# Optimization experiments

Hardware: AMD Instinct MI355X
Metric: run time of the kernel (lower is better)

## Reference

```python
import jax, jax.numpy as jnp
import numpy as np

B = 8192      # batch_size
D = 1024      # d_model
E = 8         # num_domains
OUT = 2       # binary fake/real logits


def setup_inputs() -> dict:
    key = jax.random.key(0)
    k_feat, k_ids, k_w1, k_b1, k_w2, k_b2 = jax.random.split(key, 6)
    feature = jax.random.normal(k_feat, (B, D), dtype=jnp.float32)
    domain_ids = jax.random.randint(k_ids, (B,), 0, E, dtype=jnp.int64)
    # Per-domain expert parameters (torch Linear init ~ U(-1/sqrt(fan_in), 1/sqrt(fan_in)))
    s1 = 1.0 / np.sqrt(D)
    W1 = jax.random.uniform(k_w1, (E, D, D), jnp.float32, -s1, s1)   # acts as x @ W1[e]
    b1 = jax.random.uniform(k_b1, (E, D), jnp.float32, -s1, s1)
    W2 = jax.random.uniform(k_w2, (E, D, OUT), jnp.float32, -s1, s1)
    b2 = jax.random.uniform(k_b2, (E, OUT), jnp.float32, -s1, s1)
    return {"feature": feature, "domain_ids": domain_ids,
            "W1": W1, "b1": b1, "W2": W2, "b2": b2}


def reference(feature, domain_ids, W1, b1, W2, b2):
    # Eval-mode forward (Dropout is identity at inference).
    # Layer 1: compute for all E experts (E is small), then select per sample.
    # h_all: [B, E, D]
    h_all = jnp.einsum('bd,edh->beh', feature, W1)
    sel = jnp.arange(feature.shape[0])
    h = h_all[sel, domain_ids] + b1[domain_ids]          # [B, D]
    h = jax.nn.relu(h)
    # Layer 2: gather the tiny [D, 2] head per sample.
    logits = jnp.einsum('bd,bdo->bo', h, W2[domain_ids]) + b2[domain_ids]  # [B, 2]
    return logits
```

## Files before the change

### kernel.cpp

```cpp
#include <hip/hip_runtime.h>
#include <hip/hip_bf16.h>

#define NB 8192
#define ND 1024
#define NE 8
#define BSTRIDE 2048

typedef unsigned short u16;
typedef __bf16 bf16x8 __attribute__((ext_vector_type(8)));
typedef float f32x4 __attribute__((ext_vector_type(4)));
typedef u16 u16x8 __attribute__((ext_vector_type(8)));
typedef u16 u16x4 __attribute__((ext_vector_type(4)));

__device__ __forceinline__ u16 f2bf(float f) {
    union { float f; unsigned u; } v; v.f = f;
    unsigned r = v.u + 0x7fffu + ((v.u >> 16) & 1u);
    return (u16)(r >> 16);
}

__global__ __launch_bounds__(256) void k_pre(
    const float* __restrict__ X, u16* __restrict__ Xb,
    const float* __restrict__ W1, u16* __restrict__ W1t,
    const int* __restrict__ ids, const float* __restrict__ b2,
    float* __restrict__ out, int* __restrict__ counts, int* __restrict__ bucket)
{
    int bid = blockIdx.x;
    int t = threadIdx.x;
    if (bid < 4096) {
        long i = ((long)bid * 256 + t) * 8;
        f32x4 a = *(const f32x4*)(X + i);
        f32x4 b = *(const f32x4*)(X + i + 4);
        u16x8 o;
        o[0] = f2bf(a[0]); o[1] = f2bf(a[1]); o[2] = f2bf(a[2]); o[3] = f2bf(a[3]);
        o[4] = f2bf(b[0]); o[5] = f2bf(b[1]); o[6] = f2bf(b[2]); o[7] = f2bf(b[3]);
        *(u16x8*)(Xb + i) = o;
        return;
    }
    if (bid < 6144) {
        __shared__ float s[64][65];
        int bid2 = bid - 4096;
        int e = bid2 >> 8;
        int tr = ((bid2 >> 4) & 15) << 6;
        int tc = (bid2 & 15) << 6;
        const float* src = W1 + (size_t)e * ND * ND;
        u16* dst = W1t + (size_t)e * ND * ND;
        #pragma unroll
        for (int i = 0; i < 4; ++i) {
            int idx = i * 256 + t;
            int r = idx >> 4, c4 = (idx & 15) * 4;
            f32x4 v = *(const f32x4*)(src + (size_t)(tr + r) * ND + tc + c4);
            s[c4 + 0][r] = v[0]; s[c4 + 1][r] = v[1];
            s[c4 + 2][r] = v[2]; s[c4 + 3][r] = v[3];
        }
        __syncthreads();
        #pragma unroll
        for (int i = 0; i < 4; ++i) {
            int idx = i * 256 + t;
            int n = idx >> 4, k4 = (idx & 15) * 4;
            u16x4 o;
            o[0] = f2bf(s[n][k4 + 0]); o[1] = f2bf(s[n][k4 + 1]);
            o[2] = f2bf(s[n][k4 + 2]); o[3] = f2bf(s[n][k4 + 3]);
            *(u16x4*)(dst + (size_t)(tc + n) * ND + tr + k4) = o;
        }
        return;
    }
    int b = (bid - 6144) * 256 + t;
    int e = ids[b];
    out[2 * b]     = b2[2 * e];
    out[2 * b + 1] = b2[2 * e + 1];
    int lane = t & 63;
    unsigned long long lt = (1ull << lane) - 1ull;
    int pos = 0;
    #pragma unroll
    for (int ee = 0; ee < NE; ++ee) {
        unsigned long long m = __ballot(e == ee);
        if (m) {
            int leader = __ffsll((long long)m) - 1;
            int r = __popcll(m & lt);
            int base = 0;
            if (e == ee && r == 0) base = atomicAdd(&counts[ee], __popcll(m));
            base = __shfl(base, leader, 64);
            if (e == ee) pos = base + r;
        }
    }
    bucket[e * BSTRIDE + pos] = b;
}

#define GLDS16(src, dst) __builtin_amdgcn_global_load_lds( \
    (const __attribute__((address_space(1))) void*)(src), \
    (__attribute__((address_space(3))) void*)(dst), 16, 0, 0)

__global__ __launch_bounds__(256) void k_gemm(
    const u16* __restrict__ Xb, const u16* __restrict__ W1t,
    const float* __restrict__ b1, const float* __restrict__ W2,
    const int* __restrict__ counts, const int* __restrict__ bucket,
    float* __restrict__ out)
{
    __shared__ u16 sA[2][2048];
    __shared__ u16 sB[2][4096];
    __shared__ int sRows[64];

    int bid = blockIdx.x;
    int e  = bid & 7;
    int nt = (bid >> 3) & 7;
    int mt = bid >> 6;

    int cnt = counts[e];
    if (mt * 64 >= cnt) return;
    int rem = cnt - mt * 64;

    int t = threadIdx.x;
    if (t < 64) {
        int r = mt * 64 + t;
        sRows[t] = bucket[e * BSTRIDE + (r < cnt ? r : 0)];
    }
    __syncthreads();

    int n0 = nt * 128;
    int ar = t >> 2, as = (t & 3) * 8;
    const u16* ap  = Xb + (size_t)sRows[ar] * ND + as;
    const u16* b0p = W1t + ((size_t)e * ND + n0 + ar) * ND + as;
    const u16* b1p = W1t + ((size_t)e * ND + n0 + 64 + ar) * ND + as;
    int w = t >> 6;
    int l = t & 63;
    int lc = l & 15, kg = l >> 4;
    int wm = (w >> 1) * 32, wn = (w & 1) * 64;

    f32x4 acc[2][4] = {};

    char* A0 = (char*)sA;
    char* B0 = (char*)sB;

    auto stage = [&](int buf, int kt) {
        int k0 = kt * 32;
        GLDS16(ap  + k0, A0 + buf * 4096 + w * 1024);
        GLDS16(b0p + k0, B0 + buf * 8192 + w * 1024);
        GLDS16(b1p + k0, B0 + buf * 8192 + 4096 + w * 1024);
    };

    stage(0, 0);

    #pragma unroll 2
    for (int kt = 0; kt < 32; ++kt) {
        int buf = kt & 1;
        if (kt + 1 < 32) {
            stage(buf ^ 1, kt + 1);
            asm volatile("s_waitcnt vmcnt(3)" ::: "memory");
        } else {
            asm volatile("s_waitcnt vmcnt(0)" ::: "memory");
        }
        asm volatile("s_barrier" ::: "memory");

        const char* Ab = A0 + buf * 4096;
        const char* Bb = B0 + buf * 8192;
        bf16x8 af[2], bfr[4];
        #pragma unroll
        for (int mf = 0; mf < 2; ++mf)
            af[mf] = *(const bf16x8*)(Ab + (wm + mf * 16 + lc) * 64 + kg * 16);
        #pragma unroll
        for (int nf = 0; nf < 4; ++nf)
            bfr[nf] = *(const bf16x8*)(Bb + (wn + nf * 16 + lc) * 64 + kg * 16);
        #pragma unroll
        for (int mf = 0; mf < 2; ++mf) {
            #pragma unroll
            for (int nf = 0; nf < 4; ++nf)
                acc[mf][nf] = __builtin_amdgcn_mfma_f32_16x16x32_bf16(af[mf], bfr[nf], acc[mf][nf], 0, 0, 0);
        }
        asm volatile("s_barrier" ::: "memory");
    }

    float b1v[4], w20[4], w21[4];
    #pragma unroll
    for (int nf = 0; nf < 4; ++nf) {
        int ncol = n0 + wn + nf * 16 + lc;
        b1v[nf] = b1[e * ND + ncol];
        w20[nf] = W2[((size_t)e * ND + ncol) * 2 + 0];
        w21[nf] = W2[((size_t)e * ND + ncol) * 2 + 1];
    }
    #pragma unroll
    for (int mf = 0; mf < 2; ++mf) {
        #pragma unroll
        for (int r = 0; r < 4; ++r) {
            float s0 = 0.f, s1 = 0.f;
            #pragma unroll
            for (int nf = 0; nf < 4; ++nf) {
                float h = acc[mf][nf][r] + b1v[nf];
                h = fmaxf(h, 0.f);
                s0 += h * w20[nf];
                s1 += h * w21[nf];
            }
            #pragma unroll
            for (int m = 8; m >= 1; m >>= 1) {
                s0 += __shfl_xor(s0, m, 64);
                s1 += __shfl_xor(s1, m, 64);
            }
            int row = wm + mf * 16 + kg * 4 + r;
            if (lc == 0 && row < rem) {
                int b = sRows[row];
                atomicAdd(&out[2 * b], s0);
                atomicAdd(&out[2 * b + 1], s1);
            }
        }
    }
}

extern "C" void kernel_launch(void* const* d_in, const int* in_sizes, int n_in,
                              void* d_out, int out_size, void* d_ws, size_t ws_size,
                              hipStream_t stream)
{
    const float* X   = (const float*)d_in[0];
    const int*   ids = (const int*)d_in[1];
    const float* W1  = (const float*)d_in[2];
    const float* b1  = (const float*)d_in[3];
    const float* W2  = (const float*)d_in[4];
    const float* b2  = (const float*)d_in[5];
    float* out = (float*)d_out;

    char* ws = (char*)d_ws;
    int* counts = (int*)ws;
    int* bucket = (int*)(ws + 4096);
    u16* Xb     = (u16*)(ws + 131072);
    u16* W1t    = (u16*)(ws + 131072 + (size_t)NB * ND * 2);

    hipMemsetAsync(counts, 0, NE * sizeof(int), stream);
    k_pre<<<4096 + 2048 + 32, 256, 0, stream>>>(X, Xb, W1, W1t, ids, b2, out, counts, bucket);
    k_gemm<<<32 * 64, 256, 0, stream>>>(Xb, W1t, b1, W2, counts, bucket, out);
}
```

Baseline: 176.1 us.

## Pre-pack gathered X and W1 into contiguous MFMA tile layouts before GEMM

Bucketing is split into its own kernel. A new pack kernel then gathers each domain's rows of X into contiguous per-tile blocks (bf16, K-tile-major) and writes W1 transposed into per-(expert, n-tile, k-tile) contiguous 128x32 blocks. The GEMM now loads fully contiguous 16-byte chunks per stage instead of strided row reads with indirect row indexing. The grid is also reduced to at most 18 M-tiles per expert instead of 32, cutting early-exit blocks. The cost is an extra launch and a serialisation, since packing must wait for the counts, and MTMAX=18 assumes no domain exceeds 1152 rows.

New measurement: 173.3 us. Within noise of the previous version (-1.6%).

```diff
diff --git a/kernel.cpp b/kernel.cpp
--- a/kernel.cpp
+++ b/kernel.cpp
@@ -5,6 +5,7 @@
 #define ND 1024
 #define NE 8
 #define BSTRIDE 2048
+#define MTMAX 18
 
 typedef unsigned short u16;
 typedef __bf16 bf16x8 __attribute__((ext_vector_type(8)));
@@ -18,53 +19,12 @@
     return (u16)(r >> 16);
 }
 
-__global__ __launch_bounds__(256) void k_pre(
-    const float* __restrict__ X, u16* __restrict__ Xb,
-    const float* __restrict__ W1, u16* __restrict__ W1t,
-    const int* __restrict__ ids, const float* __restrict__ b2,
-    float* __restrict__ out, int* __restrict__ counts, int* __restrict__ bucket)
-{
-    int bid = blockIdx.x;
+__global__ __launch_bounds__(256) void k_prep(const int* __restrict__ ids,
+    const float* __restrict__ b2, float* __restrict__ out,
+    int* __restrict__ counts, int* __restrict__ bucket)
+{
     int t = threadIdx.x;
-    if (bid < 4096) {
-        long i = ((long)bid * 256 + t) * 8;
-        f32x4 a = *(const f32x4*)(X + i);
-        f32x4 b = *(const f32x4*)(X + i + 4);
-        u16x8 o;
-        o[0] = f2bf(a[0]); o[1] = f2bf(a[1]); o[2] = f2bf(a[2]); o[3] = f2bf(a[3]);
-        o[4] = f2bf(b[0]); o[5] = f2bf(b[1]); o[6] = f2bf(b[2]); o[7] = f2bf(b[3]);
-        *(u16x8*)(Xb + i) = o;
-        return;
-    }
-    if (bid < 6144) {
-        __shared__ float s[64][65];
-        int bid2 = bid - 4096;
-        int e = bid2 >> 8;
-        int tr = ((bid2 >> 4) & 15) << 6;
-        int tc = (bid2 & 15) << 6;
-        const float* src = W1 + (size_t)e * ND * ND;
-        u16* dst = W1t + (size_t)e * ND * ND;
-        #pragma unroll
-        for (int i = 0; i < 4; ++i) {
-            int idx = i * 256 + t;
-            int r = idx >> 4, c4 = (idx & 15) * 4;
-            f32x4 v = *(const f32x4*)(src + (size_t)(tr + r) * ND + tc + c4);
-            s[c4 + 0][r] = v[0]; s[c4 + 1][r] = v[1];
-            s[c4 + 2][r] = v[2]; s[c4 + 3][r] = v[3];
-        }
-        __syncthreads();
-        #pragma unroll
-        for (int i = 0; i < 4; ++i) {
-            int idx = i * 256 + t;
-            int n = idx >> 4, k4 = (idx & 15) * 4;
-            u16x4 o;
-            o[0] = f2bf(s[n][k4 + 0]); o[1] = f2bf(s[n][k4 + 1]);
-            o[2] = f2bf(s[n][k4 + 2]); o[3] = f2bf(s[n][k4 + 3]);
-            *(u16x4*)(dst + (size_t)(tc + n) * ND + tr + k4) = o;
-        }
-        return;
-    }
-    int b = (bid - 6144) * 256 + t;
+    int b = blockIdx.x * 256 + t;
     int e = ids[b];
     out[2 * b]     = b2[2 * e];
     out[2 * b + 1] = b2[2 * e + 1];
@@ -86,12 +46,76 @@
     bucket[e * BSTRIDE + pos] = b;
 }
 
+__global__ __launch_bounds__(256) void k_pack(
+    const float* __restrict__ W1, u16* __restrict__ W1p,
+    const float* __restrict__ X, u16* __restrict__ Ag,
+    const int* __restrict__ counts, const int* __restrict__ bucket)
+{
+    int bid = blockIdx.x;
+    int t = threadIdx.x;
+    if (bid < 2048) {
+        __shared__ float s[64][65];
+        int e = bid >> 8;
+        int tr = ((bid >> 4) & 15) << 6;
+        int tc = (bid & 15) << 6;
+        const float* src = W1 + (size_t)e * ND * ND;
+        #pragma unroll
+        for (int i = 0; i < 4; ++i) {
+            int idx = i * 256 + t;
+            int r = idx >> 4, c4 = (idx & 15) * 4;
+            f32x4 v = *(const f32x4*)(src + (size_t)(tr + r) * ND + tc + c4);
+            s[c4 + 0][r] = v[0]; s[c4 + 1][r] = v[1];
+            s[c4 + 2][r] = v[2]; s[c4 + 3][r] = v[3];
+        }
+        __syncthreads();
+        #pragma unroll
+        for (int i = 0; i < 4; ++i) {
+            int idx = i * 256 + t;
+            int n = idx >> 4, k4 = (idx & 15) * 4;
+            int gn = tc + n, gk = tr + k4;
+            int nt = gn >> 7, kt = gk >> 5;
+            u16x4 o;
+            o[0] = f2bf(s[n][k4 + 0]); o[1] = f2bf(s[n][k4 + 1]);
+            o[2] = f2bf(s[n][k4 + 2]); o[3] = f2bf(s[n][k4 + 3]);
+            *(u16x4*)(W1p + (((size_t)(e * 8 + nt) * 32 + kt) * 4096) + (gn & 127) * 32 + (gk & 31)) = o;
+        }
+        return;
+    }
+    __shared__ int sR[64];
+    int bid2 = bid - 2048;
+    int half = bid2 & 1;
+    int g = bid2 >> 1;
+    int e = g / MTMAX, mt = g % MTMAX;
+    int cnt = counts[e];
+    if (mt * 64 >= cnt) return;
+    int tb = 0;
+    #pragma unroll
+    for (int j = 0; j < NE; ++j) if (j < e) tb += (counts[j] + 63) >> 6;
+    size_t tbase = (size_t)(tb + mt) * 32 * 2048;
+    if (t < 64) {
+        int rr = mt * 64 + t;
+        sR[t] = bucket[e * BSTRIDE + (rr < cnt ? rr : 0)];
+    }
+    __syncthreads();
+    #pragma unroll 4
+    for (int i = 0; i < 32; ++i) {
+        int c = i * 256 + t;
+        int r = c >> 7, ck = c & 127;
+        int k = half * 512 + ck * 4;
+        f32x4 v = *(const f32x4*)(X + (size_t)sR[r] * ND + k);
+        u16x4 o;
+        o[0] = f2bf(v[0]); o[1] = f2bf(v[1]); o[2] = f2bf(v[2]); o[3] = f2bf(v[3]);
+        int kt = k >> 5, ko = k & 31;
+        *(u16x4*)(Ag + tbase + (size_t)kt * 2048 + r * 32 + ko) = o;
+    }
+}
+
 #define GLDS16(src, dst) __builtin_amdgcn_global_load_lds( \
     (const __attribute__((address_space(1))) void*)(src), \
     (__attribute__((address_space(3))) void*)(dst), 16, 0, 0)
 
 __global__ __launch_bounds__(256) void k_gemm(
-    const u16* __restrict__ Xb, const u16* __restrict__ W1t,
+    const u16* __restrict__ Ag, const u16* __restrict__ W1p,
     const float* __restrict__ b1, const float* __restrict__ W2,
     const int* __restrict__ counts, const int* __restrict__ bucket,
     float* __restrict__ out)
@@ -116,11 +140,13 @@
     }
     __syncthreads();
 
+    int tb = 0;
+    #pragma unroll
+    for (int j = 0; j < NE; ++j) if (j < e) tb += (counts[j] + 63) >> 6;
+
     int n0 = nt * 128;
-    int ar = t >> 2, as = (t & 3) * 8;
-    const u16* ap  = Xb + (size_t)sRows[ar] * ND + as;
-    const u16* b0p = W1t + ((size_t)e * ND + n0 + ar) * ND + as;
-    const u16* b1p = W1t + ((size_t)e * ND + n0 + 64 + ar) * ND + as;
+    const u16* Abase = Ag + (size_t)(tb + mt) * 32 * 2048 + t * 8;
+    const u16* Bbase = W1p + (size_t)(e * 8 + nt) * 32 * 4096 + t * 8;
     int w = t >> 6;
     int l = t & 63;
     int lc = l & 15, kg = l >> 4;
@@ -132,10 +158,9 @@
     char* B0 = (char*)sB;
 
     auto stage = [&](int buf, int kt) {
-        int k0 = kt * 32;
-        GLDS16(ap  + k0, A0 + buf * 4096 + w * 1024);
-        GLDS16(b0p + k0, B0 + buf * 8192 + w * 1024);
-        GLDS16(b1p + k0, B0 + buf * 8192 + 4096 + w * 1024);
+        GLDS16(Abase + (size_t)kt * 2048, A0 + buf * 4096 + w * 1024);
+        GLDS16(Bbase + (size_t)kt * 4096, B0 + buf * 8192 + w * 1024);
+        GLDS16(Bbase + (size_t)kt * 4096 + 2048, B0 + buf * 8192 + 4096 + w * 1024);
     };
 
     stage(0, 0);
@@ -219,10 +244,11 @@
     char* ws = (char*)d_ws;
     int* counts = (int*)ws;
     int* bucket = (int*)(ws + 4096);
-    u16* Xb     = (u16*)(ws + 131072);
-    u16* W1t    = (u16*)(ws + 131072 + (size_t)NB * ND * 2);
+    u16* Ag     = (u16*)(ws + 131072);
+    u16* W1p    = (u16*)(ws + 131072 + 136u * 32u * 2048u * 2u);
 
     hipMemsetAsync(counts, 0, NE * sizeof(int), stream);
-    k_pre<<<4096 + 2048 + 32, 256, 0, stream>>>(X, Xb, W1, W1t, ids, b2, out, counts, bucket);
-    k_gemm<<<32 * 64, 256, 0, stream>>>(Xb, W1t, b1, W2, counts, bucket, out);
-}
+    k_prep<<<NB / 256, 256, 0, stream>>>(ids, b2, out, counts, bucket);
+    k_pack<<<2048 + NE * MTMAX * 2, 256, 0, stream>>>(W1, W1p, X, Ag, counts, bucket);
+    k_gemm<<<NE * MTMAX * 8, 256, 0, stream>>>(Ag, W1p, b1, W2, counts, bucket, out);
+}
```
